# Performance work log

Hardware: AMD Instinct MI355X
Metric: run time of the kernel (lower is better)

The kernel has to match this reference:

```python
import jax, jax.numpy as jnp
import numpy as np

B, N, DIM, H, DH = 4, 2048, 512, 8, 64  # patches_num == N (required by the math)
INNER = H * DH
SCALE = DH ** -0.5


def setup_inputs() -> dict:
    key = jax.random.key(0)
    ks = jax.random.split(key, 6)
    s = lambda fan_in: 1.0 / np.sqrt(fan_in)
    return {
        "x": jax.random.normal(ks[0], (B, N, DIM), dtype=jnp.float32),
        "w_qkfv": jax.random.normal(ks[1], (DIM, 4 * INNER), dtype=jnp.float32) * s(DIM),
        "w_scales": jax.random.normal(ks[2], (DH, N), dtype=jnp.float32) * s(DH),
        "b_scales": jax.random.normal(ks[3], (N,), dtype=jnp.float32) * s(DH),
        "w_out": jax.random.normal(ks[4], (INNER, DIM), dtype=jnp.float32) * s(INNER),
        "b_out": jax.random.normal(ks[5], (DIM,), dtype=jnp.float32) * s(INNER),
    }


def reference(x, w_qkfv, w_scales, b_scales, w_out, b_out):
    # Fused qkfv projection: [B,N,4*INNER]
    qkfv = x @ w_qkfv
    q, k, f, v = jnp.split(qkfv, 4, axis=-1)
    split_heads = lambda t: t.reshape(B, N, H, DH).transpose(0, 2, 1, 3)  # b h n d
    q, k, f, v = map(split_heads, (q, k, f, v))

    # q @ k^T * scale -> [b,h,n,n]
    scores = jnp.einsum("bhid,bhjd->bhij", q, k) * SCALE
    attn = jax.nn.softmax(scores, axis=-1)

    # f^T @ v -> [b,h,d,d], then Linear(dim_head -> patches_num) -> [b,h,d,n]
    poss_value = jnp.einsum("bhnd,bhne->bhde", f, v)
    poss_value = poss_value @ w_scales + b_scales  # [b,h,d,n]

    # attn @ poss_value^T -> [b,h,n,d]
    out = jnp.einsum("bhij,bhdj->bhid", attn, poss_value)
    out = out.transpose(0, 2, 1, 3).reshape(B, N, INNER)  # b n (h d)

    # to_out (dropout=0 / eval mode -> identity)
    return out @ w_out + b_out
```

## Files before the change

kernel.cpp:

```cpp
#include <hip/hip_runtime.h>
#include <stdint.h>

#define N_SEQ 2048
#define QKFV_COLS 2048

typedef __attribute__((ext_vector_type(8))) __bf16 bf16x8;
typedef __attribute__((ext_vector_type(4))) __bf16 bf16x4;
typedef __attribute__((ext_vector_type(4))) float f32x4;
typedef __attribute__((ext_vector_type(16))) float f32x16;

#if __has_builtin(__builtin_amdgcn_exp2f)
#define EXP2(x) __builtin_amdgcn_exp2f(x)
#else
#define EXP2(x) exp2f(x)
#endif

__device__ __forceinline__ f32x4 mfma16(bf16x8 a, bf16x8 b, f32x4 c) {
  return __builtin_amdgcn_mfma_f32_16x16x32_bf16(a, b, c, 0, 0, 0);
}
__device__ __forceinline__ f32x16 mfma32(bf16x8 a, bf16x8 b, f32x16 c) {
  return __builtin_amdgcn_mfma_f32_32x32x16_bf16(a, b, c, 0, 0, 0);
}

__device__ __forceinline__ void glds16(const void* g, void* l) {
  __builtin_amdgcn_global_load_lds(
      (__attribute__((address_space(1))) uint32_t*)(uintptr_t)g,
      (__attribute__((address_space(3))) uint32_t*)l, 16, 0, 0);
}

__global__ __launch_bounds__(256) void cast_bf16_kernel(const float* __restrict__ in,
                                                        __bf16* __restrict__ out, int n8) {
  int i = blockIdx.x * 256 + threadIdx.x;
  if (i >= n8) return;
  const float* p = in + (size_t)i * 8;
  bf16x8 o;
#pragma unroll
  for (int j = 0; j < 8; ++j) o[j] = (__bf16)p[j];
  *(bf16x8*)(out + (size_t)i * 8) = o;
}

__global__ __launch_bounds__(256) void transpose_cast_kernel(const float* __restrict__ in,
                                                             __bf16* __restrict__ out,
                                                             int R, int C) {
  int i = blockIdx.x * 256 + threadIdx.x;
  int nchunks = C * (R / 8);
  if (i >= nchunks) return;
  int c = i / (R / 8);
  int r0 = (i % (R / 8)) * 8;
  bf16x8 o;
#pragma unroll
  for (int j = 0; j < 8; ++j) o[j] = (__bf16)in[(size_t)(r0 + j) * C + c];
  *(bf16x8*)(out + (size_t)c * R + r0) = o;
}

template<typename OUT_T, bool BIAS>
__global__ __launch_bounds__(256) void gemm_bt_kernel(const __bf16* __restrict__ A,
                                                      const __bf16* __restrict__ Bt,
                                                      OUT_T* __restrict__ C,
                                                      const float* __restrict__ bias,
                                                      int M, int N, int K) {
  __shared__ alignas(16) __bf16 As[128 * 32];
  __shared__ alignas(16) __bf16 Bs[128 * 32];
  const int t = threadIdx.x;
  const int w = t >> 6;
  const int lane = t & 63;
  const int ln = lane & 15;
  const int hi8 = (lane >> 4) * 8;
  const int g4 = (lane >> 4) * 4;
  const int wr = w >> 1, wc = w & 1;
  const int m0 = blockIdx.x * 128, n0 = blockIdx.y * 128;

  f32x4 acc[4][4];
#pragma unroll
  for (int m = 0; m < 4; ++m)
#pragma unroll
    for (int n = 0; n < 4; ++n) acc[m][n] = (f32x4){0.f, 0.f, 0.f, 0.f};

  const int nk = K >> 5;
  for (int kt = 0; kt < nk; ++kt) {
    const int k0 = kt << 5;
#pragma unroll
    for (int i = 0; i < 2; ++i) {
      int c = i * 256 + t;
      int r = c >> 2, cc = c & 3;
      glds16(A + (size_t)(m0 + r) * K + k0 + cc * 8, &As[(i * 256 + w * 64) * 8]);
      glds16(Bt + (size_t)(n0 + r) * K + k0 + cc * 8, &Bs[(i * 256 + w * 64) * 8]);
    }
    __syncthreads();
    bf16x8 af[4], bfr[4];
#pragma unroll
    for (int m = 0; m < 4; ++m) af[m] = *(const bf16x8*)&As[(wr * 64 + m * 16 + ln) * 32 + hi8];
#pragma unroll
    for (int n = 0; n < 4; ++n) bfr[n] = *(const bf16x8*)&Bs[(wc * 64 + n * 16 + ln) * 32 + hi8];
#pragma unroll
    for (int m = 0; m < 4; ++m)
#pragma unroll
      for (int n = 0; n < 4; ++n) acc[m][n] = mfma16(af[m], bfr[n], acc[m][n]);
    __syncthreads();
  }

#pragma unroll
  for (int m = 0; m < 4; ++m)
#pragma unroll
    for (int n = 0; n < 4; ++n) {
      int col = n0 + wc * 64 + n * 16 + ln;
      float bv = BIAS ? bias[col] : 0.f;
#pragma unroll
      for (int r = 0; r < 4; ++r) {
        int row = m0 + wr * 64 + m * 16 + g4 + r;
        C[(size_t)row * N + col] = (OUT_T)(acc[m][n][r] + bv);
      }
    }
}

__global__ __launch_bounds__(512, 2) void gemm256_kernel(const __bf16* __restrict__ A,
                                                         const __bf16* __restrict__ Bt,
                                                         __bf16* __restrict__ C,
                                                         __bf16* __restrict__ fT,
                                                         __bf16* __restrict__ vT) {
  __shared__ alignas(16) __bf16 Ab[2][256 * 64];
  __shared__ alignas(16) __bf16 Bb[2][256 * 64];
  const int K = 512, N = 2048;
  const int t = threadIdx.x;
  const int w = t >> 6;
  const int lane = t & 63;
  const int l15 = lane & 15;
  const int q4 = lane >> 4;
  const int g4 = q4 * 4;
  const int wr = w >> 2, wc = w & 3;
  const int bid = blockIdx.x;
  const int wg = (bid & 7) * 32 + (bid >> 3);
  const int m0 = (wg & 31) * 256;
  const int n0 = (wg >> 5) * 256;

  const __bf16* srcA[4];
  const __bf16* srcB[4];
#pragma unroll
  for (int c = 0; c < 4; ++c) {
    int s = c * 512 + t;
    int r = s >> 3, u = (s & 7) ^ (r & 7);
    srcA[c] = A + (size_t)(m0 + r) * K + u * 8;
    srcB[c] = Bt + (size_t)(n0 + r) * K + u * 8;
  }

  f32x4 acc[8][4];
#pragma unroll
  for (int m = 0; m < 8; ++m)
#pragma unroll
    for (int n = 0; n < 4; ++n) acc[m][n] = (f32x4){0.f, 0.f, 0.f, 0.f};

  const int sA = l15 & 7;

#pragma unroll
  for (int c = 0; c < 4; ++c) {
    glds16(srcA[c], &Ab[0][(c * 512 + w * 64) * 8]);
    glds16(srcB[c], &Bb[0][(c * 512 + w * 64) * 8]);
  }

  const int nkt = K >> 6;
  for (int kt = 0; kt < nkt; ++kt) {
    const int cur = kt & 1;
    asm volatile("s_waitcnt vmcnt(0)" ::: "memory");
    __builtin_amdgcn_s_barrier();
    const int knext = (kt + 1) << 6;
    const bool pf = (kt + 1) < nkt;
#pragma unroll
    for (int mh = 0; mh < 2; ++mh) {
      bf16x8 a[4][2];
#pragma unroll
      for (int nh = 0; nh < 2; ++nh) {
        if (nh == 0) {
#pragma unroll
          for (int mm = 0; mm < 4; ++mm) {
            const int R = wr * 128 + (mh * 4 + mm) * 16 + l15;
#pragma unroll
            for (int ks = 0; ks < 2; ++ks)
              a[mm][ks] = *(const bf16x8*)&Ab[cur][R * 64 + (((ks * 4 + q4) ^ sA) * 8)];
          }
        }
        bf16x8 bfrag[2][2];
#pragma unroll
        for (int nn = 0; nn < 2; ++nn) {
          const int R = wc * 64 + (nh * 2 + nn) * 16 + l15;
#pragma unroll
          for (int ks = 0; ks < 2; ++ks)
            bfrag[nn][ks] = *(const bf16x8*)&Bb[cur][R * 64 + (((ks * 4 + q4) ^ sA) * 8)];
        }
        if (pf) {
          const int c = mh * 2 + nh;
          glds16(srcA[c] + knext, &Ab[cur ^ 1][(c * 512 + w * 64) * 8]);
          glds16(srcB[c] + knext, &Bb[cur ^ 1][(c * 512 + w * 64) * 8]);
        }
        __builtin_amdgcn_s_barrier();
        asm volatile("s_waitcnt lgkmcnt(0)" ::: "memory");
        __builtin_amdgcn_sched_barrier(0);
        __builtin_amdgcn_s_setprio(1);
#pragma unroll
        for (int mm = 0; mm < 4; ++mm)
#pragma unroll
          for (int nn = 0; nn < 2; ++nn)
#pragma unroll
            for (int ks = 0; ks < 2; ++ks)
              acc[mh * 4 + mm][nh * 2 + nn] =
                  mfma16(a[mm][ks], bfrag[nn][ks], acc[mh * 4 + mm][nh * 2 + nn]);
        __builtin_amdgcn_s_setprio(0);
        __builtin_amdgcn_s_barrier();
      }
    }
  }

  if (n0 < 1024) {
#pragma unroll
    for (int m = 0; m < 8; ++m)
#pragma unroll
      for (int n = 0; n < 4; ++n) {
        const int col = n0 + wc * 64 + n * 16 + l15;
        const int row = m0 + wr * 128 + m * 16 + g4;
#pragma unroll
        for (int r = 0; r < 4; ++r)
          C[(size_t)(row + r) * N + col] = (__bf16)acc[m][n][r];
      }
  } else {
    __bf16* T = (n0 < 1536) ? fT : vT;
    const int cbase = (n0 < 1536) ? 1024 : 1536;
#pragma unroll
    for (int m = 0; m < 8; ++m)
#pragma unroll
      for (int n = 0; n < 4; ++n) {
        const int hc = n0 + wc * 64 + n * 16 + l15 - cbase;
        const int h = hc >> 6, d = hc & 63;
        const int row = m0 + wr * 128 + m * 16 + g4;
        const int b = row >> 11, nl = row & 2047;
        bf16x4 pk;
#pragma unroll
        for (int r = 0; r < 4; ++r) pk[r] = (__bf16)acc[m][n][r];
        *(bf16x4*)&T[(size_t)((b * 8 + h) * 64 + d) * 2048 + nl] = pk;
      }
  }
}

__global__ __launch_bounds__(256) void fvmm_kernel(const __bf16* __restrict__ fT,
                                                   const __bf16* __restrict__ vT,
                                                   float* __restrict__ fvp) {
  __shared__ alignas(16) __bf16 As[2 * 8192];
  __shared__ alignas(16) __bf16 Bs[2 * 8192];
  const int t = threadIdx.x;
  const int w = t >> 6;
  const int lane = t & 63;
  const int l15 = lane & 15;
  const int q4 = lane >> 4;
  const int g4 = q4 * 4;
  const int sl = blockIdx.x;
  const int bh = blockIdx.y;
  const int k0 = sl * 256;
  const __bf16* A = fT + (size_t)bh * 131072 + k0;
  const __bf16* B = vT + (size_t)bh * 131072 + k0;

#pragma unroll
  for (int kt = 0; kt < 2; ++kt)
#pragma unroll
    for (int c = 0; c < 4; ++c) {
      int slot = c * 256 + t;
      int r = slot >> 4, u = (slot & 15) ^ (r & 7);
      glds16(A + (size_t)r * 2048 + kt * 128 + u * 8, &As[kt * 8192 + (c * 256 + w * 64) * 8]);
      glds16(B + (size_t)r * 2048 + kt * 128 + u * 8, &Bs[kt * 8192 + (c * 256 + w * 64) * 8]);
    }
  asm volatile("s_waitcnt vmcnt(0)" ::: "memory");
  __syncthreads();

  f32x4 acc[4];
#pragma unroll
  for (int nb = 0; nb < 4; ++nb) acc[nb] = (f32x4){0.f, 0.f, 0.f, 0.f};
  const int arow = w * 16 + l15;
#pragma unroll
  for (int ks = 0; ks < 8; ++ks) {
    const int kt = ks >> 2;
    const int ku = (ks & 3) * 4 + q4;
    bf16x8 a = *(const bf16x8*)&As[kt * 8192 + arow * 128 + ((ku ^ (arow & 7)) * 8)];
#pragma unroll
    for (int nb = 0; nb < 4; ++nb) {
      const int br = nb * 16 + l15;
      bf16x8 bb = *(const bf16x8*)&Bs[kt * 8192 + br * 128 + ((ku ^ (br & 7)) * 8)];
      acc[nb] = mfma16(a, bb, acc[nb]);
    }
  }
  float* dst = fvp + (size_t)(sl * 32 + bh) * 4096;
#pragma unroll
  for (int nb = 0; nb < 4; ++nb)
#pragma unroll
    for (int r = 0; r < 4; ++r)
      dst[(w * 16 + g4 + r) * 64 + nb * 16 + l15] = acc[nb][r];
}

__global__ __launch_bounds__(256) void pvmat2_kernel(const float* __restrict__ fvp,
                                                     const __bf16* __restrict__ wscT,
                                                     const float* __restrict__ bsc,
                                                     __bf16* __restrict__ pvm) {
  __shared__ alignas(16) __bf16 fs[64 * 72];
  __shared__ alignas(16) __bf16 Ws[128 * 64];
  const int t = threadIdx.x;
  const int w = t >> 6;
  const int lane = t & 63;
  const int l15 = lane & 15;
  const int q4 = lane >> 4;
  const int g4 = q4 * 4;
  const int bh = blockIdx.y;
  const int j0 = blockIdx.x * 128;

#pragma unroll
  for (int c = 0; c < 4; ++c) {
    int slot = c * 256 + t;
    int r = slot >> 3, u = (slot & 7) ^ (r & 7);
    glds16(wscT + (size_t)(j0 + r) * 64 + u * 8, &Ws[(c * 256 + w * 64) * 8]);
  }
#pragma unroll
  for (int qq = 0; qq < 4; ++qq) {
    int idx = t * 16 + qq * 4;
    f32x4 s = (f32x4){0.f, 0.f, 0.f, 0.f};
#pragma unroll
    for (int sl = 0; sl < 8; ++sl)
      s += *(const f32x4*)&fvp[(size_t)(sl * 32 + bh) * 4096 + idx];
    bf16x4 pk;
#pragma unroll
    for (int e = 0; e < 4; ++e) pk[e] = (__bf16)s[e];
    *(bf16x4*)&fs[(idx >> 6) * 72 + (idx & 63)] = pk;
  }
  asm volatile("s_waitcnt vmcnt(0)" ::: "memory");
  __syncthreads();

  f32x4 acc[8];
#pragma unroll
  for (int nb = 0; nb < 8; ++nb) {
    float bv = bsc[j0 + nb * 16 + l15];
    acc[nb] = (f32x4){bv, bv, bv, bv};
  }
  const int arow = w * 16 + l15;
#pragma unroll
  for (int ks = 0; ks < 2; ++ks) {
    bf16x8 a = *(const bf16x8*)&fs[arow * 72 + ks * 32 + q4 * 8];
#pragma unroll
    for (int nb = 0; nb < 8; ++nb) {
      const int jr = nb * 16 + l15;
      bf16x8 bb = *(const bf16x8*)&Ws[jr * 64 + (((ks * 4 + q4) ^ (jr & 7)) * 8)];
      acc[nb] = mfma16(a, bb, acc[nb]);
    }
  }
  __bf16* dst = pvm + (size_t)bh * 131072 + (size_t)j0;
#pragma unroll
  for (int nb = 0; nb < 8; ++nb)
#pragma unroll
    for (int r = 0; r < 4; ++r)
      dst[(size_t)(w * 16 + g4 + r) * 2048 + nb * 16 + l15] = (__bf16)acc[nb][r];
}

__global__ __launch_bounds__(512, 4) void attn_kernel(const __bf16* __restrict__ qkfv,
                                                      const __bf16* __restrict__ pvm,
                                                      __bf16* __restrict__ obuf) {
  __shared__ alignas(16) char smem[65536];
  __bf16* Kb = (__bf16*)smem;
  __bf16* Vb = (__bf16*)(smem + 32768);
  const int t = threadIdx.x;
  const int w = t >> 6;
  const int g = w >> 2;
  const int wq = w & 3;
  const int lane = t & 63;
  const int ln = lane & 31;
  const int hi = lane >> 5;
  const int p = blockIdx.x;
  const int bh = (p & 7) * 4 + ((p >> 3) & 3);
  const int iblk = p >> 5;
  const int b = bh >> 3, h = bh & 7;
  const int irow = iblk * 128 + wq * 32 + ln;
  const float K1 = 0.18033688f;
  const int swz = ln & 7;

  bf16x8 q[4];
  const __bf16* qrow = qkfv + (size_t)(b * N_SEQ + irow) * QKFV_COLS + h * 64 + hi * 8;
#pragma unroll
  for (int kf = 0; kf < 4; ++kf) {
    bf16x8 raw = *(const bf16x8*)(qrow + kf * 16);
#pragma unroll
    for (int e = 0; e < 8; ++e) q[kf][e] = (__bf16)((float)raw[e] * K1);
  }

  const int tg = t & 255;
  const __bf16* ksrc[2];
  const __bf16* vsrc[2];
#pragma unroll
  for (int it = 0; it < 2; ++it) {
    int s = it * 256 + tg;
    int r = s >> 3;
    int u = (s & 7) ^ (r & 7);
    ksrc[it] = qkfv + (size_t)(b * N_SEQ + g * 1024 + r) * QKFV_COLS + 512 + h * 64 + u * 8;
    vsrc[it] = pvm + ((size_t)bh * 64 + r) * 2048 + g * 1024 + u * 8;
  }

  auto stage = [&](int buf, int jt) {
#pragma unroll
    for (int it = 0; it < 2; ++it) {
      glds16(ksrc[it] + ((size_t)jt << 17), &Kb[(g * 2 + buf) * 4096 + (it * 256 + wq * 64) * 8]);
      glds16(vsrc[it] + jt * 64, &Vb[(g * 2 + buf) * 4096 + (it * 256 + wq * 64) * 8]);
    }
  };

  f32x16 o0, o1;
#pragma unroll
  for (int e = 0; e < 16; ++e) { o0[e] = 0.f; o1[e] = 0.f; }
  float lrl = 0.f;

  stage(0, 0);

  for (int jt = 0; jt < 16; ++jt) {
    asm volatile("s_waitcnt vmcnt(0)" ::: "memory");
    __builtin_amdgcn_s_barrier();
    if (jt < 15) stage((jt & 1) ^ 1, jt + 1);
    const int kc = (g * 2 + (jt & 1)) * 4096;

    f32x16 s0, s1;
#pragma unroll
    for (int e = 0; e < 16; ++e) { s0[e] = 0.f; s1[e] = 0.f; }
    __builtin_amdgcn_s_setprio(1);
#pragma unroll
    for (int kf = 0; kf < 4; ++kf) {
      bf16x8 k0 = *(const bf16x8*)&Kb[kc + (ln) * 64 + (((2 * kf + hi) ^ swz) * 8)];
      bf16x8 k1 = *(const bf16x8*)&Kb[kc + (32 + ln) * 64 + (((2 * kf + hi) ^ swz) * 8)];
      s0 = mfma32(k0, q[kf], s0);
      s1 = mfma32(k1, q[kf], s1);
    }
    __builtin_amdgcn_s_setprio(0);

#pragma unroll
    for (int e = 0; e < 16; ++e) s0[e] = EXP2(s0[e]);
#pragma unroll
    for (int e = 0; e < 16; ++e) s1[e] = EXP2(s1[e]);
    float a8[8];
#pragma unroll
    for (int e = 0; e < 8; ++e)
      a8[e] = (s0[e] + s0[e + 8]) + (s1[e] + s1[e + 8]);
    lrl += ((a8[0] + a8[4]) + (a8[1] + a8[5])) + ((a8[2] + a8[6]) + (a8[3] + a8[7]));

    bf16x8 pa[4];
#pragma unroll
    for (int kk = 0; kk < 4; ++kk) {
      const f32x16& sf = (kk < 2) ? s0 : s1;
      const int rb = (kk & 1) * 8;
      uint32_t a0, a1, b0, b1;
      asm("v_cvt_pk_bf16_f32 %0, %1, %2" : "=v"(a0) : "v"(sf[rb + 0]), "v"(sf[rb + 1]));
      asm("v_cvt_pk_bf16_f32 %0, %1, %2" : "=v"(a1) : "v"(sf[rb + 2]), "v"(sf[rb + 3]));
      asm("v_cvt_pk_bf16_f32 %0, %1, %2" : "=v"(b0) : "v"(sf[rb + 4]), "v"(sf[rb + 5]));
      asm("v_cvt_pk_bf16_f32 %0, %1, %2" : "=v"(b1) : "v"(sf[rb + 6]), "v"(sf[rb + 7]));
      asm("v_permlane32_swap_b32 %0, %1" : "+v"(a0), "+v"(b0));
      asm("v_permlane32_swap_b32 %0, %1" : "+v"(a1), "+v"(b1));
      union { uint32_t u[4]; bf16x8 v; } cv;
      cv.u[0] = a0; cv.u[1] = a1; cv.u[2] = b0; cv.u[3] = b1;
      pa[kk] = cv.v;
    }

    __builtin_amdgcn_s_setprio(1);
#pragma unroll
    for (int kk = 0; kk < 4; ++kk) {
      bf16x8 v0 = *(const bf16x8*)&Vb[kc + (ln) * 64 + (((2 * kk + hi) ^ swz) * 8)];
      bf16x8 v1 = *(const bf16x8*)&Vb[kc + (32 + ln) * 64 + (((2 * kk + hi) ^ swz) * 8)];
      o0 = mfma32(v0, pa[kk], o0);
      o1 = mfma32(v1, pa[kk], o1);
    }
    __builtin_amdgcn_s_setprio(0);
  }

  lrl += __shfl_xor(lrl, 32);

  __syncthreads();
  float* Om = (float*)smem;
  if (w >= 4) {
    const int base = ((w - 4) * 64 + lane) * 33;
#pragma unroll
    for (int e = 0; e < 16; ++e) { Om[base + e] = o0[e]; Om[base + 16 + e] = o1[e]; }
    Om[base + 32] = lrl;
  }
  __syncthreads();
  if (w < 4) {
    const int base = (w * 64 + lane) * 33;
#pragma unroll
    for (int e = 0; e < 16; ++e) { o0[e] += Om[base + e]; o1[e] += Om[base + 16 + e]; }
    lrl += Om[base + 32];

    const float inv = 1.0f / lrl;
    const size_t orow = (size_t)(b * N_SEQ + irow) * 512 + h * 64;
#pragma unroll
    for (int df = 0; df < 2; ++df) {
      const f32x16& oo = df ? o1 : o0;
#pragma unroll
      for (int gg = 0; gg < 4; ++gg) {
        bf16x4 pk;
#pragma unroll
        for (int e = 0; e < 4; ++e) pk[e] = (__bf16)(oo[gg * 4 + e] * inv);
        *(bf16x4*)(obuf + orow + df * 32 + gg * 8 + hi * 4) = pk;
      }
    }
  }
}

extern "C" void kernel_launch(void* const* d_in, const int* in_sizes, int n_in,
                              void* d_out, int out_size, void* d_ws, size_t ws_size,
                              hipStream_t stream) {
  (void)in_sizes; (void)n_in; (void)out_size; (void)ws_size;
  const float* x   = (const float*)d_in[0];
  const float* wqk = (const float*)d_in[1];
  const float* wsc = (const float*)d_in[2];
  const float* bsc = (const float*)d_in[3];
  const float* wo  = (const float*)d_in[4];
  const float* bo  = (const float*)d_in[5];
  float* out = (float*)d_out;

  char* p = (char*)d_ws;
  __bf16* xbf  = (__bf16*)p;  p += (size_t)8192 * 512 * 2;
  __bf16* wqT  = (__bf16*)p;  p += (size_t)2048 * 512 * 2;
  __bf16* woT  = (__bf16*)p;  p += (size_t)512 * 512 * 2;
  __bf16* wscT = (__bf16*)p;  p += (size_t)2048 * 64 * 2;
  __bf16* qkfv = (__bf16*)p;  p += (size_t)8192 * 2048 * 2;
  __bf16* pvm  = (__bf16*)p;  p += (size_t)32 * 64 * 2048 * 2;
  __bf16* obuf = (__bf16*)p;  p += (size_t)8192 * 512 * 2;
  float* fvp = (float*)xbf;
  __bf16* fT = obuf;
  __bf16* vT = pvm;

  cast_bf16_kernel<<<dim3(2048), dim3(256), 0, stream>>>(x, xbf, 8192 * 512 / 8);
  transpose_cast_kernel<<<dim3(512), dim3(256), 0, stream>>>(wqk, wqT, 512, 2048);
  transpose_cast_kernel<<<dim3(128), dim3(256), 0, stream>>>(wo, woT, 512, 512);
  transpose_cast_kernel<<<dim3(64), dim3(256), 0, stream>>>(wsc, wscT, 64, 2048);
  gemm256_kernel<<<dim3(256), dim3(512), 0, stream>>>(xbf, wqT, qkfv, fT, vT);
  fvmm_kernel<<<dim3(8, 32), dim3(256), 0, stream>>>(fT, vT, fvp);
  pvmat2_kernel<<<dim3(16, 32), dim3(256), 0, stream>>>(fvp, wscT, bsc, pvm);
  attn_kernel<<<dim3(512), dim3(512), 0, stream>>>(qkfv, pvm, obuf);
  gemm_bt_kernel<float, true><<<dim3(64, 4), dim3(256), 0, stream>>>(obuf, woT, out, bo, 8192, 512, 512);
}
```

Measured before the change: 126.8 us.

## Fuse prep casts into one tiled kernel and retile QKFV and output GEMMs

The four cast and transpose launches become a single prep kernel, and the weight transposes now go through a shared-memory tile so both global reads and writes are coalesced. The QKFV projection GEMM moves from 256x256 tiles with K-step 64 to 128x256 tiles with K-step 32, which doubles the block count for better CU coverage and cuts shared memory to allow more blocks per CU. The output projection uses smaller 128x64 tiles with 512 threads, swizzled LDS and more blocks. The trade-off is less data reuse per tile and more barrier steps in the GEMMs.

```diff
diff --git a/kernel.cpp b/kernel.cpp
--- a/kernel.cpp
+++ b/kernel.cpp
@@ -28,98 +28,63 @@
       (__attribute__((address_space(3))) uint32_t*)l, 16, 0, 0);
 }
 
-__global__ __launch_bounds__(256) void cast_bf16_kernel(const float* __restrict__ in,
-                                                        __bf16* __restrict__ out, int n8) {
-  int i = blockIdx.x * 256 + threadIdx.x;
-  if (i >= n8) return;
-  const float* p = in + (size_t)i * 8;
-  bf16x8 o;
-#pragma unroll
-  for (int j = 0; j < 8; ++j) o[j] = (__bf16)p[j];
-  *(bf16x8*)(out + (size_t)i * 8) = o;
-}
-
-__global__ __launch_bounds__(256) void transpose_cast_kernel(const float* __restrict__ in,
-                                                             __bf16* __restrict__ out,
-                                                             int R, int C) {
-  int i = blockIdx.x * 256 + threadIdx.x;
-  int nchunks = C * (R / 8);
-  if (i >= nchunks) return;
-  int c = i / (R / 8);
-  int r0 = (i % (R / 8)) * 8;
-  bf16x8 o;
-#pragma unroll
-  for (int j = 0; j < 8; ++j) o[j] = (__bf16)in[(size_t)(r0 + j) * C + c];
-  *(bf16x8*)(out + (size_t)c * R + r0) = o;
-}
-
-template<typename OUT_T, bool BIAS>
-__global__ __launch_bounds__(256) void gemm_bt_kernel(const __bf16* __restrict__ A,
-                                                      const __bf16* __restrict__ Bt,
-                                                      OUT_T* __restrict__ C,
-                                                      const float* __restrict__ bias,
-                                                      int M, int N, int K) {
-  __shared__ alignas(16) __bf16 As[128 * 32];
-  __shared__ alignas(16) __bf16 Bs[128 * 32];
+__global__ __launch_bounds__(256) void prep_kernel(const float* __restrict__ x,
+                                                   __bf16* __restrict__ xbf,
+                                                   const float* __restrict__ wqk,
+                                                   __bf16* __restrict__ wqT,
+                                                   const float* __restrict__ wo,
+                                                   __bf16* __restrict__ woT,
+                                                   const float* __restrict__ wsc,
+                                                   __bf16* __restrict__ wscT) {
   const int t = threadIdx.x;
-  const int w = t >> 6;
-  const int lane = t & 63;
-  const int ln = lane & 15;
-  const int hi8 = (lane >> 4) * 8;
-  const int g4 = (lane >> 4) * 4;
-  const int wr = w >> 1, wc = w & 1;
-  const int m0 = blockIdx.x * 128, n0 = blockIdx.y * 128;
-
-  f32x4 acc[4][4];
-#pragma unroll
-  for (int m = 0; m < 4; ++m)
-#pragma unroll
-    for (int n = 0; n < 4; ++n) acc[m][n] = (f32x4){0.f, 0.f, 0.f, 0.f};
-
-  const int nk = K >> 5;
-  for (int kt = 0; kt < nk; ++kt) {
-    const int k0 = kt << 5;
-#pragma unroll
-    for (int i = 0; i < 2; ++i) {
-      int c = i * 256 + t;
-      int r = c >> 2, cc = c & 3;
-      glds16(A + (size_t)(m0 + r) * K + k0 + cc * 8, &As[(i * 256 + w * 64) * 8]);
-      glds16(Bt + (size_t)(n0 + r) * K + k0 + cc * 8, &Bs[(i * 256 + w * 64) * 8]);
-    }
-    __syncthreads();
-    bf16x8 af[4], bfr[4];
-#pragma unroll
-    for (int m = 0; m < 4; ++m) af[m] = *(const bf16x8*)&As[(wr * 64 + m * 16 + ln) * 32 + hi8];
-#pragma unroll
-    for (int n = 0; n < 4; ++n) bfr[n] = *(const bf16x8*)&Bs[(wc * 64 + n * 16 + ln) * 32 + hi8];
-#pragma unroll
-    for (int m = 0; m < 4; ++m)
-#pragma unroll
-      for (int n = 0; n < 4; ++n) acc[m][n] = mfma16(af[m], bfr[n], acc[m][n]);
-    __syncthreads();
-  }
-
-#pragma unroll
-  for (int m = 0; m < 4; ++m)
-#pragma unroll
-    for (int n = 0; n < 4; ++n) {
-      int col = n0 + wc * 64 + n * 16 + ln;
-      float bv = BIAS ? bias[col] : 0.f;
-#pragma unroll
-      for (int r = 0; r < 4; ++r) {
-        int row = m0 + wr * 64 + m * 16 + g4 + r;
-        C[(size_t)row * N + col] = (OUT_T)(acc[m][n][r] + bv);
-      }
-    }
-}
-
-__global__ __launch_bounds__(512, 2) void gemm256_kernel(const __bf16* __restrict__ A,
-                                                         const __bf16* __restrict__ Bt,
-                                                         __bf16* __restrict__ C,
-                                                         __bf16* __restrict__ fT,
-                                                         __bf16* __restrict__ vT) {
-  __shared__ alignas(16) __bf16 Ab[2][256 * 64];
-  __shared__ alignas(16) __bf16 Bb[2][256 * 64];
+  int bid = blockIdx.x;
+  if (bid < 2048) {
+    size_t i = (size_t)bid * 2048 + t * 8;
+    const float* p = x + i;
+    bf16x8 o;
+#pragma unroll
+    for (int j = 0; j < 8; ++j) o[j] = (__bf16)p[j];
+    *(bf16x8*)(xbf + i) = o;
+    return;
+  }
+  bid -= 2048;
+  const float* in;
+  __bf16* outp;
+  int R, C, rt, ct;
+  if (bid < 256) { in = wqk; outp = wqT; R = 512; C = 2048; rt = bid >> 5; ct = bid & 31; }
+  else if (bid < 320) { int b2 = bid - 256; in = wo; outp = woT; R = 512; C = 512; rt = b2 >> 3; ct = b2 & 7; }
+  else { int b2 = bid - 320; in = wsc; outp = wscT; R = 64; C = 2048; rt = 0; ct = b2; }
+  __shared__ __bf16 tile[64][72];
+  const int r0 = rt * 64, c0 = ct * 64;
+  {
+    const int r = t >> 2, cq = (t & 3) * 16;
+    const float* src = in + (size_t)(r0 + r) * C + c0 + cq;
+#pragma unroll
+    for (int q = 0; q < 4; ++q) {
+      f32x4 v = *(const f32x4*)(src + q * 4);
+#pragma unroll
+      for (int e = 0; e < 4; ++e) tile[r][cq + q * 4 + e] = (__bf16)v[e];
+    }
+  }
+  __syncthreads();
+  {
+    const int c = t >> 2, rq = (t & 3) * 16;
+    __bf16* dst = outp + (size_t)(c0 + c) * R + r0 + rq;
+    bf16x8 o0, o1;
+#pragma unroll
+    for (int j = 0; j < 8; ++j) { o0[j] = tile[rq + j][c]; o1[j] = tile[rq + 8 + j][c]; }
+    *(bf16x8*)dst = o0;
+    *(bf16x8*)(dst + 8) = o1;
+  }
+}
+
+__global__ __launch_bounds__(512, 4) void gemm_qkfv_kernel(const __bf16* __restrict__ A,
+                                                           const __bf16* __restrict__ Bt,
+                                                           __bf16* __restrict__ C,
+                                                           __bf16* __restrict__ fT,
+                                                           __bf16* __restrict__ vT) {
+  __shared__ alignas(16) __bf16 Ab[2][128 * 32];
+  __shared__ alignas(16) __bf16 Bb[2][256 * 32];
   const int K = 512, N = 2048;
   const int t = threadIdx.x;
   const int w = t >> 6;
@@ -129,93 +94,68 @@
   const int g4 = q4 * 4;
   const int wr = w >> 2, wc = w & 3;
   const int bid = blockIdx.x;
-  const int wg = (bid & 7) * 32 + (bid >> 3);
-  const int m0 = (wg & 31) * 256;
-  const int n0 = (wg >> 5) * 256;
-
-  const __bf16* srcA[4];
-  const __bf16* srcB[4];
-#pragma unroll
-  for (int c = 0; c < 4; ++c) {
-    int s = c * 512 + t;
-    int r = s >> 3, u = (s & 7) ^ (r & 7);
-    srcA[c] = A + (size_t)(m0 + r) * K + u * 8;
+  const int n0 = (bid & 7) * 256;
+  const int m0 = (bid >> 3) * 128;
+
+  const __bf16* srcA;
+  const __bf16* srcB[2];
+  {
+    int s = t, r = s >> 2, u = (s & 3) ^ (r & 3);
+    srcA = A + (size_t)(m0 + r) * K + u * 8;
+  }
+#pragma unroll
+  for (int c = 0; c < 2; ++c) {
+    int s = c * 512 + t, r = s >> 2, u = (s & 3) ^ (r & 3);
     srcB[c] = Bt + (size_t)(n0 + r) * K + u * 8;
   }
 
-  f32x4 acc[8][4];
-#pragma unroll
-  for (int m = 0; m < 8; ++m)
+  f32x4 acc[4][4];
+#pragma unroll
+  for (int m = 0; m < 4; ++m)
 #pragma unroll
     for (int n = 0; n < 4; ++n) acc[m][n] = (f32x4){0.f, 0.f, 0.f, 0.f};
 
-  const int sA = l15 & 7;
-
-#pragma unroll
-  for (int c = 0; c < 4; ++c) {
-    glds16(srcA[c], &Ab[0][(c * 512 + w * 64) * 8]);
-    glds16(srcB[c], &Bb[0][(c * 512 + w * 64) * 8]);
-  }
-
-  const int nkt = K >> 6;
-  for (int kt = 0; kt < nkt; ++kt) {
+  glds16(srcA, &Ab[0][t * 8]);
+  glds16(srcB[0], &Bb[0][t * 8]);
+  glds16(srcB[1], &Bb[0][(512 + t) * 8]);
+
+  for (int kt = 0; kt < 16; ++kt) {
     const int cur = kt & 1;
     asm volatile("s_waitcnt vmcnt(0)" ::: "memory");
     __builtin_amdgcn_s_barrier();
-    const int knext = (kt + 1) << 6;
-    const bool pf = (kt + 1) < nkt;
-#pragma unroll
-    for (int mh = 0; mh < 2; ++mh) {
-      bf16x8 a[4][2];
-#pragma unroll
-      for (int nh = 0; nh < 2; ++nh) {
-        if (nh == 0) {
-#pragma unroll
-          for (int mm = 0; mm < 4; ++mm) {
-            const int R = wr * 128 + (mh * 4 + mm) * 16 + l15;
-#pragma unroll
-            for (int ks = 0; ks < 2; ++ks)
-              a[mm][ks] = *(const bf16x8*)&Ab[cur][R * 64 + (((ks * 4 + q4) ^ sA) * 8)];
-          }
-        }
-        bf16x8 bfrag[2][2];
-#pragma unroll
-        for (int nn = 0; nn < 2; ++nn) {
-          const int R = wc * 64 + (nh * 2 + nn) * 16 + l15;
-#pragma unroll
-          for (int ks = 0; ks < 2; ++ks)
-            bfrag[nn][ks] = *(const bf16x8*)&Bb[cur][R * 64 + (((ks * 4 + q4) ^ sA) * 8)];
-        }
-        if (pf) {
-          const int c = mh * 2 + nh;
-          glds16(srcA[c] + knext, &Ab[cur ^ 1][(c * 512 + w * 64) * 8]);
-          glds16(srcB[c] + knext, &Bb[cur ^ 1][(c * 512 + w * 64) * 8]);
-        }
-        __builtin_amdgcn_s_barrier();
-        asm volatile("s_waitcnt lgkmcnt(0)" ::: "memory");
-        __builtin_amdgcn_sched_barrier(0);
-        __builtin_amdgcn_s_setprio(1);
-#pragma unroll
-        for (int mm = 0; mm < 4; ++mm)
-#pragma unroll
-          for (int nn = 0; nn < 2; ++nn)
-#pragma unroll
-            for (int ks = 0; ks < 2; ++ks)
-              acc[mh * 4 + mm][nh * 2 + nn] =
-                  mfma16(a[mm][ks], bfrag[nn][ks], acc[mh * 4 + mm][nh * 2 + nn]);
-        __builtin_amdgcn_s_setprio(0);
-        __builtin_amdgcn_s_barrier();
-      }
-    }
+    if (kt < 15) {
+      const int k0 = (kt + 1) * 32;
+      glds16(srcA + k0, &Ab[cur ^ 1][t * 8]);
+      glds16(srcB[0] + k0, &Bb[cur ^ 1][t * 8]);
+      glds16(srcB[1] + k0, &Bb[cur ^ 1][(512 + t) * 8]);
+    }
+    bf16x8 af[4], bf[4];
+#pragma unroll
+    for (int m = 0; m < 4; ++m) {
+      const int R = wr * 64 + m * 16 + l15;
+      af[m] = *(const bf16x8*)&Ab[cur][R * 32 + ((q4 ^ (R & 3)) * 8)];
+    }
+#pragma unroll
+    for (int n = 0; n < 4; ++n) {
+      const int R = wc * 64 + n * 16 + l15;
+      bf[n] = *(const bf16x8*)&Bb[cur][R * 32 + ((q4 ^ (R & 3)) * 8)];
+    }
+    __builtin_amdgcn_s_setprio(1);
+#pragma unroll
+    for (int m = 0; m < 4; ++m)
+#pragma unroll
+      for (int n = 0; n < 4; ++n) acc[m][n] = mfma16(af[m], bf[n], acc[m][n]);
+    __builtin_amdgcn_s_setprio(0);
+    __builtin_amdgcn_s_barrier();
   }
 
   if (n0 < 1024) {
 #pragma unroll
-    for (int m = 0; m < 8; ++m)
+    for (int m = 0; m < 4; ++m)
 #pragma unroll
       for (int n = 0; n < 4; ++n) {
         const int col = n0 + wc * 64 + n * 16 + l15;
-        const int row = m0 + wr * 128 + m * 16 + g4;
+        const int row = m0 + wr * 64 + m * 16 + g4;
 #pragma unroll
         for (int r = 0; r < 4; ++r)
           C[(size_t)(row + r) * N + col] = (__bf16)acc[m][n][r];
@@ -224,12 +164,12 @@
     __bf16* T = (n0 < 1536) ? fT : vT;
     const int cbase = (n0 < 1536) ? 1024 : 1536;
 #pragma unroll
-    for (int m = 0; m < 8; ++m)
+    for (int m = 0; m < 4; ++m)
 #pragma unroll
       for (int n = 0; n < 4; ++n) {
         const int hc = n0 + wc * 64 + n * 16 + l15 - cbase;
         const int h = hc >> 6, d = hc & 63;
-        const int row = m0 + wr * 128 + m * 16 + g4;
+        const int row = m0 + wr * 64 + m * 16 + g4;
         const int b = row >> 11, nl = row & 2047;
         bf16x4 pk;
 #pragma unroll
@@ -237,6 +177,72 @@
         *(bf16x4*)&T[(size_t)((b * 8 + h) * 64 + d) * 2048 + nl] = pk;
       }
   }
+}
+
+__global__ __launch_bounds__(512, 4) void gemm_out_kernel(const __bf16* __restrict__ A,
+                                                          const __bf16* __restrict__ Bt,
+                                                          float* __restrict__ out,
+                                                          const float* __restrict__ bias) {
+  __shared__ alignas(16) __bf16 As[128 * 32];
+  __shared__ alignas(16) __bf16 Bs[64 * 32];
+  const int K = 512, N = 512;
+  const int t = threadIdx.x;
+  const int w = t >> 6;
+  const int lane = t & 63;
+  const int l15 = lane & 15;
+  const int q4 = lane >> 4;
+  const int g4 = q4 * 4;
+  const int wr = w >> 1, wc = w & 1;
+  const int m0 = blockIdx.x * 128, n0 = blockIdx.y * 64;
+
+  const __bf16* srcA;
+  const __bf16* srcB;
+  {
+    int s = t, r = s >> 2, u = (s & 3) ^ (r & 3);
+    srcA = A + (size_t)(m0 + r) * K + u * 8;
+    srcB = Bt + (size_t)(n0 + (r & 63)) * K + u * 8;
+  }
+
+  f32x4 acc[2][2];
+#pragma unroll
+  for (int m = 0; m < 2; ++m)
+#pragma unroll
+    for (int n = 0; n < 2; ++n) acc[m][n] = (f32x4){0.f, 0.f, 0.f, 0.f};
+
+  for (int kt = 0; kt < 16; ++kt) {
+    const int k0 = kt * 32;
+    glds16(srcA + k0, &As[t * 8]);
+    if (t < 256) glds16(srcB + k0, &Bs[t * 8]);
+    __syncthreads();
+    bf16x8 af[2], bf[2];
+#pragma unroll
+    for (int m = 0; m < 2; ++m) {
+      const int R = wr * 32 + m * 16 + l15;
+      af[m] = *(const bf16x8*)&As[R * 32 + ((q4 ^ (R & 3)) * 8)];
+    }
+#pragma unroll
+    for (int n = 0; n < 2; ++n) {
+      const int R = wc * 32 + n * 16 + l15;
+      bf[n] = *(const bf16x8*)&Bs[R * 32 + ((q4 ^ (R & 3)) * 8)];
+    }
+#pragma unroll
+    for (int m = 0; m < 2; ++m)
+#pragma unroll
+      for (int n = 0; n < 2; ++n) acc[m][n] = mfma16(af[m], bf[n], acc[m][n]);
+    __syncthreads();
+  }
+
+#pragma unroll
+  for (int m = 0; m < 2; ++m)
+#pragma unroll
+    for (int n = 0; n < 2; ++n) {
+      const int col = n0 + wc * 32 + n * 16 + l15;
+      const float bv = bias[col];
+      const int row = m0 + wr * 32 + m * 16 + g4;
+#pragma unroll
+      for (int r = 0; r < 4; ++r)
+        out[(size_t)(row + r) * N + col] = acc[m][n][r] + bv;
+    }
 }
 
 __global__ __launch_bounds__(256) void fvmm_kernel(const __bf16* __restrict__ fT,
@@ -524,13 +530,10 @@
   __bf16* fT = obuf;
   __bf16* vT = pvm;
 
-  cast_bf16_kernel<<<dim3(2048), dim3(256), 0, stream>>>(x, xbf, 8192 * 512 / 8);
-  transpose_cast_kernel<<<dim3(512), dim3(256), 0, stream>>>(wqk, wqT, 512, 2048);
-  transpose_cast_kernel<<<dim3(128), dim3(256), 0, stream>>>(wo, woT, 512, 512);
-  transpose_cast_kernel<<<dim3(64), dim3(256), 0, stream>>>(wsc, wscT, 64, 2048);
-  gemm256_kernel<<<dim3(256), dim3(512), 0, stream>>>(xbf, wqT, qkfv, fT, vT);
+  prep_kernel<<<dim3(2400), dim3(256), 0, stream>>>(x, xbf, wqk, wqT, wo, woT, wsc, wscT);
+  gemm_qkfv_kernel<<<dim3(512), dim3(512), 0, stream>>>(xbf, wqT, qkfv, fT, vT);
   fvmm_kernel<<<dim3(8, 32), dim3(256), 0, stream>>>(fT, vT, fvp);
   pvmat2_kernel<<<dim3(16, 32), dim3(256), 0, stream>>>(fvp, wscT, bsc, pvm);
   attn_kernel<<<dim3(512), dim3(512), 0, stream>>>(qkfv, pvm, obuf);
-  gemm_bt_kernel<float, true><<<dim3(64, 4), dim3(256), 0, stream>>>(obuf, woT, out, bo, 8192, 512, 512);
-}
+  gemm_out_kernel<<<dim3(64, 8), dim3(512), 0, stream>>>(obuf, woT, out, bo);
+}
```

New measurement: 111.1 us. 1.14x faster.
